# Kernel optimization log

Measured on AMD Instinct MI355X. Metric: run time of the kernel, lower is better.

Reference implementation:

```python
import jax, jax.numpy as jnp
import numpy as np

D = 1024
H = 16
DH = D // H
B = 8
T = 1024
EPS = 1e-5


def setup_inputs() -> dict:
    key = jax.random.key(0)
    ks = jax.random.split(key, 12)
    s = 0.02
    return {
        "x": jax.random.normal(ks[0], (B, T, D), dtype=jnp.float32),
        "ln1_scale": jnp.ones((D,), jnp.float32),
        "ln1_shift": jnp.zeros((D,), jnp.float32),
        "Wq": jax.random.normal(ks[1], (D, D), jnp.float32) * s,
        "Wk": jax.random.normal(ks[2], (D, D), jnp.float32) * s,
        "Wv": jax.random.normal(ks[3], (D, D), jnp.float32) * s,
        "Wo": jax.random.normal(ks[4], (D, D), jnp.float32) * s,
        "bo": jnp.zeros((D,), jnp.float32),
        "ln2_scale": jnp.ones((D,), jnp.float32),
        "ln2_shift": jnp.zeros((D,), jnp.float32),
        "W1": jax.random.normal(ks[5], (D, 4 * D), jnp.float32) * s,
        "b1": jnp.zeros((4 * D,), jnp.float32),
        "W2": jax.random.normal(ks[6], (4 * D, D), jnp.float32) * s,
        "b2": jnp.zeros((D,), jnp.float32),
    }


def _layernorm(x, scale, shift):
    mean = jnp.mean(x, axis=-1, keepdims=True)
    var = jnp.mean((x - mean) ** 2, axis=-1, keepdims=True)  # unbiased=False
    return (x - mean) * jax.lax.rsqrt(var + EPS) * scale + shift


def _gelu_tanh(x):
    c = jnp.sqrt(jnp.float32(2.0 / jnp.pi))
    return 0.5 * x * (1.0 + jnp.tanh(c * (x + 0.044715 * x ** 3)))


def reference(x, ln1_scale, ln1_shift, Wq, Wk, Wv, Wo, bo,
              ln2_scale, ln2_shift, W1, b1, W2, b2):
    b, t, d = x.shape
    x1 = _layernorm(x, ln1_scale, ln1_shift)
    # QKV projections (no bias), split heads -> (b, h, t, d_h)
    q = (x1 @ Wq).reshape(b, t, H, DH).transpose(0, 2, 1, 3)
    k = (x1 @ Wk).reshape(b, t, H, DH).transpose(0, 2, 1, 3)
    v = (x1 @ Wv).reshape(b, t, H, DH).transpose(0, 2, 1, 3)
    scores = jnp.einsum("bhqd,bhkd->bhqk", q, k) / jnp.sqrt(jnp.float32(DH))
    # original does tril then adds -inf upper-triangular mask -> standard causal mask
    causal = jnp.tril(jnp.ones((t, t), dtype=bool))
    scores = jnp.where(causal, scores, -jnp.inf)
    attn = jax.nn.softmax(scores, axis=-1)
    z = jnp.einsum("bhqk,bhkd->bhqd", attn, v)
    z = z.transpose(0, 2, 1, 3).reshape(b, t, d)
    x2 = z @ Wo + bo
    y = x2 + x
    y1 = _layernorm(y, ln2_scale, ln2_shift)
    y2 = _gelu_tanh(y1 @ W1 + b1) @ W2 + b2
    return y2 + y
```

## Files before the change

### kernel.cpp

```cpp
#include <hip/hip_runtime.h>

typedef unsigned short u16;
typedef __bf16 bf16x8 __attribute__((ext_vector_type(8)));
typedef float f32x4 __attribute__((ext_vector_type(4)));

#define D_MODEL 1024
#define NHEAD 16
#define DHEAD 64
#define BATCH 8
#define SEQ 1024
#define NROW 8192

__device__ __forceinline__ u16 f2bf(float f) {
  union { float f; unsigned int u; } a; a.f = f;
  unsigned int u = a.u;
  return (u16)((u + 0x7fffu + ((u >> 16) & 1u)) >> 16);
}

__device__ __forceinline__ float gelu_f(float x) {
  float y = 0.79788456080286535588f * (x + 0.044715f * x * x * x);
  return x / (1.0f + __expf(-2.0f * y));
}

__device__ __forceinline__ void async16(const void* gsrc, void* ldst) {
  __builtin_amdgcn_global_load_lds((__attribute__((address_space(1))) void*)gsrc,
                                   (__attribute__((address_space(3))) void*)ldst,
                                   16, 0, 0);
}

__global__ __launch_bounds__(256)
void wconv_kernel(const float* __restrict__ W, u16* __restrict__ WT, int K, int N) {
  __shared__ float tile[32][33];
  const int tx = threadIdx.x & 31, ty = threadIdx.x >> 5;
  const int n0 = blockIdx.x * 32, k0 = blockIdx.y * 32;
#pragma unroll
  for (int r = 0; r < 4; ++r)
    tile[ty + r * 8][tx] = W[(size_t)(k0 + ty + r * 8) * N + n0 + tx];
  __syncthreads();
#pragma unroll
  for (int r = 0; r < 4; ++r)
    WT[(size_t)(n0 + ty + r * 8) * K + k0 + tx] = f2bf(tile[tx][ty + r * 8]);
}

__global__ __launch_bounds__(256)
void ln_kernel(const float* __restrict__ x, const float* __restrict__ gamma,
               const float* __restrict__ beta, u16* __restrict__ out) {
  const int row = blockIdx.x, t = threadIdx.x;
  const float4 v = ((const float4*)(x + (size_t)row * D_MODEL))[t];
  float s  = v.x + v.y + v.z + v.w;
  float s2 = v.x * v.x + v.y * v.y + v.z * v.z + v.w * v.w;
#pragma unroll
  for (int off = 32; off >= 1; off >>= 1) {
    s  += __shfl_down(s, off);
    s2 += __shfl_down(s2, off);
  }
  __shared__ float red[8];
  const int w = t >> 6, l = t & 63;
  if (l == 0) { red[w] = s; red[4 + w] = s2; }
  __syncthreads();
  s  = red[0] + red[1] + red[2] + red[3];
  s2 = red[4] + red[5] + red[6] + red[7];
  const float mean = s * (1.0f / D_MODEL);
  const float var  = s2 * (1.0f / D_MODEL) - mean * mean;
  const float inv  = rsqrtf(var + 1e-5f);
  const float4 ga = ((const float4*)gamma)[t];
  const float4 be = ((const float4*)beta)[t];
  ushort4 ov;
  ov.x = f2bf((v.x - mean) * inv * ga.x + be.x);
  ov.y = f2bf((v.y - mean) * inv * ga.y + be.y);
  ov.z = f2bf((v.z - mean) * inv * ga.z + be.z);
  ov.w = f2bf((v.w - mean) * inv * ga.w + be.w);
  ((ushort4*)out)[(size_t)row * 256 + t] = ov;
}

#define MODE_QK 0
#define MODE_VT 1
#define MODE_F32_RES 2
#define MODE_GELU 3

template <int MODE>
__global__ __launch_bounds__(256, 2)
void gemm_bt(const u16* __restrict__ A, const u16* __restrict__ BT,
             const float* __restrict__ bias, const float* __restrict__ resid,
             void* __restrict__ outp, int M, int N, int K) {
  __shared__ u16 sA[2][128 * 32];
  __shared__ u16 sB[2][128 * 32];
  const int t = threadIdx.x;
  const int w = t >> 6, l = t & 63;
  const int c = l & 15, g = l >> 4;
  const int wr = w >> 1, wc = w & 1;
  const int bm = blockIdx.x, bn = blockIdx.y;

  f32x4 acc[4][4] = {};

  const char* Ab = (const char*)(A + (size_t)bm * 128 * K);
  const char* Bb = (const char*)(BT + (size_t)bn * 128 * K);
  const size_t ldb = (size_t)K * 2;
  const int srow = t >> 2;
  const int scolb = (t & 3) * 16;
  const int ldsoff = w * 1024;

  auto stage = [&](int buf, int k0) {
#pragma unroll
    for (int i = 0; i < 2; ++i) {
      async16(Ab + (size_t)(srow + i * 64) * ldb + (size_t)k0 * 2 + scolb,
              (char*)sA[buf] + i * 4096 + ldsoff);
      async16(Bb + (size_t)(srow + i * 64) * ldb + (size_t)k0 * 2 + scolb,
              (char*)sB[buf] + i * 4096 + ldsoff);
    }
  };

  stage(0, 0);
  asm volatile("s_waitcnt vmcnt(0)" ::: "memory");
  __builtin_amdgcn_s_barrier();

  const int nt = K >> 5;
  for (int it = 0; it < nt; ++it) {
    const int cur = it & 1;
    if (it + 1 < nt) stage(cur ^ 1, (it + 1) << 5);
    bf16x8 af[4], bfr[4];
#pragma unroll
    for (int m = 0; m < 4; ++m)
      af[m] = *(const bf16x8*)&sA[cur][(wr * 64 + m * 16 + c) * 32 + g * 8];
#pragma unroll
    for (int n = 0; n < 4; ++n)
      bfr[n] = *(const bf16x8*)&sB[cur][(wc * 64 + n * 16 + c) * 32 + g * 8];
#pragma unroll
    for (int m = 0; m < 4; ++m)
#pragma unroll
      for (int n = 0; n < 4; ++n)
        acc[m][n] = __builtin_amdgcn_mfma_f32_16x16x32_bf16(af[m], bfr[n], acc[m][n], 0, 0, 0);
    asm volatile("s_waitcnt vmcnt(0)" ::: "memory");
    __builtin_amdgcn_s_barrier();
  }

#pragma unroll
  for (int m = 0; m < 4; ++m) {
    const int r0 = bm * 128 + wr * 64 + m * 16 + g * 4;
#pragma unroll
    for (int n = 0; n < 4; ++n) {
      const int cc = bn * 128 + wc * 64 + n * 16 + c;
#pragma unroll
      for (int i = 0; i < 4; ++i) {
        const int r = r0 + i;
        const float v = acc[m][n][i];
        if constexpr (MODE == MODE_QK) {
          ((u16*)outp)[(((size_t)(r >> 10) * NHEAD + (cc >> 6)) * SEQ + (r & 1023)) * DHEAD + (cc & 63)] = f2bf(v);
        } else if constexpr (MODE == MODE_VT) {
          ((u16*)outp)[(((size_t)(r >> 10) * NHEAD + (cc >> 6)) * DHEAD + (cc & 63)) * SEQ + (r & 1023)] = f2bf(v);
        } else if constexpr (MODE == MODE_F32_RES) {
          const size_t idx = (size_t)r * N + cc;
          ((float*)outp)[idx] = v + bias[cc] + resid[idx];
        } else {
          const size_t idx = (size_t)r * N + cc;
          ((u16*)outp)[idx] = f2bf(gelu_f(v + bias[cc]));
        }
      }
    }
  }
}

__global__ __launch_bounds__(256, 3)
void attn_kernel(const u16* __restrict__ q, const u16* __restrict__ k,
                 const u16* __restrict__ vT, u16* __restrict__ z) {
  __shared__ u16 sK[2][64 * 64];
  __shared__ u16 sV[2][64 * 64];
  __shared__ u16 pb[4][32 * 64];

  const int t = threadIdx.x, w = t >> 6, l = t & 63;
  const int c = l & 15, g = l >> 4;
  const int bh = blockIdx.y;
  const int qb0 = blockIdx.x * 128;
  const int qw0 = qb0 + w * 32;

  const u16* qbase = q  + (size_t)bh * SEQ * DHEAD;
  const u16* kbase = k  + (size_t)bh * SEQ * DHEAD;
  const u16* vbase = vT + (size_t)bh * DHEAD * SEQ;

  bf16x8 qf[2][2];
#pragma unroll
  for (int j = 0; j < 2; ++j)
#pragma unroll
    for (int hh = 0; hh < 2; ++hh)
      qf[j][hh] = *(const bf16x8*)&qbase[(size_t)(qw0 + j * 16 + c) * DHEAD + hh * 32 + g * 8];

  f32x4 o[4][2] = {};
  float m[2]  = {-3.0e38f, -3.0e38f};
  float ls[2] = {0.0f, 0.0f};

  const int r8 = l >> 3, ch = l & 7;
  const int sw16 = (ch ^ r8) * 16;

  auto stage = [&](int buf, int kt) {
    const int kb0 = kt * 64;
#pragma unroll
    for (int i = 0; i < 2; ++i) {
      const int row = w * 8 + i * 32 + r8;
      async16((const char*)kbase + (size_t)(kb0 + row) * 128 + sw16,
              (char*)sK[buf] + w * 1024 + i * 4096);
      async16((const char*)vbase + (size_t)row * (SEQ * 2) + (size_t)kb0 * 2 + sw16,
              (char*)sV[buf] + w * 1024 + i * 4096);
    }
  };

  const int nkt = blockIdx.x * 2 + 2;
  stage(0, 0);

  for (int kt = 0; kt < nkt; ++kt) {
    const int cur = kt & 1;
    if (kt + 1 < nkt) {
      stage(cur ^ 1, kt + 1);
      asm volatile("s_waitcnt vmcnt(4)" ::: "memory");
    } else {
      asm volatile("s_waitcnt vmcnt(0)" ::: "memory");
    }
    __builtin_amdgcn_s_barrier();

    const int kb0 = kt * 64;
    if (kb0 < qw0 + 32) {
      const u16* sKc = sK[cur];
      const u16* sVc = sV[cur];
      const int cx = c & 7;

      f32x4 st[4][2];
#pragma unroll
      for (int s = 0; s < 4; ++s) {
        const int row = s * 16 + c;
        bf16x8 kf0 = *(const bf16x8*)&sKc[row * 64 + ((0 + g) ^ cx) * 8];
        bf16x8 kf1 = *(const bf16x8*)&sKc[row * 64 + ((4 + g) ^ cx) * 8];
#pragma unroll
        for (int j = 0; j < 2; ++j) {
          f32x4 z4 = {};
          z4 = __builtin_amdgcn_mfma_f32_16x16x32_bf16(kf0, qf[j][0], z4, 0, 0, 0);
          z4 = __builtin_amdgcn_mfma_f32_16x16x32_bf16(kf1, qf[j][1], z4, 0, 0, 0);
          st[s][j] = z4;
        }
      }

      const bool full = (kb0 + 64 <= qw0 + 1);
      float tmax[2] = {-3.0e38f, -3.0e38f};
#pragma unroll
      for (int s = 0; s < 4; ++s)
#pragma unroll
        for (int j = 0; j < 2; ++j)
#pragma unroll
          for (int i = 0; i < 4; ++i) {
            float vsc = st[s][j][i] * 0.125f;
            if (!full) {
              const int key = kb0 + s * 16 + g * 4 + i;
              vsc = (key <= qw0 + j * 16 + c) ? vsc : -1.0e30f;
            }
            st[s][j][i] = vsc;
            tmax[j] = fmaxf(tmax[j], vsc);
          }
#pragma unroll
      for (int j = 0; j < 2; ++j) {
        tmax[j] = fmaxf(tmax[j], __shfl_xor(tmax[j], 16));
        tmax[j] = fmaxf(tmax[j], __shfl_xor(tmax[j], 32));
      }
      float mnew[2], sc[2], psum[2];
#pragma unroll
      for (int j = 0; j < 2; ++j) {
        mnew[j] = fmaxf(m[j], tmax[j]);
        sc[j]   = __expf(m[j] - mnew[j]);
        psum[j] = 0.0f;
      }
#pragma unroll
      for (int s = 0; s < 4; ++s)
#pragma unroll
        for (int j = 0; j < 2; ++j)
#pragma unroll
          for (int i = 0; i < 4; ++i) {
            const float pv = __expf(st[s][j][i] - mnew[j]);
            st[s][j][i] = pv;
            psum[j] += pv;
          }
#pragma unroll
      for (int j = 0; j < 2; ++j) {
        psum[j] += __shfl_xor(psum[j], 16);
        psum[j] += __shfl_xor(psum[j], 32);
        ls[j] = ls[j] * sc[j] + psum[j];
        m[j]  = mnew[j];
#pragma unroll
        for (int d = 0; d < 4; ++d) o[d][j] = o[d][j] * sc[j];
      }

      u16* pw = pb[w];
#pragma unroll
      for (int s = 0; s < 4; ++s)
#pragma unroll
        for (int j = 0; j < 2; ++j) {
          const int row = j * 16 + c;
          const int swz = (s * 2 + (g >> 1)) ^ cx;
          ushort4 pv4;
          pv4.x = f2bf(st[s][j][0]); pv4.y = f2bf(st[s][j][1]);
          pv4.z = f2bf(st[s][j][2]); pv4.w = f2bf(st[s][j][3]);
          *(ushort4*)&pw[row * 64 + swz * 8 + (g & 1) * 4] = pv4;
        }

      bf16x8 pf[2][2];
#pragma unroll
      for (int j = 0; j < 2; ++j)
#pragma unroll
        for (int ks = 0; ks < 2; ++ks)
          pf[j][ks] = *(const bf16x8*)&pw[(j * 16 + c) * 64 + ((ks * 4 + g) ^ cx) * 8];

#pragma unroll
      for (int d = 0; d < 4; ++d) {
        const int vrow = d * 16 + c;
#pragma unroll
        for (int ks = 0; ks < 2; ++ks) {
          bf16x8 vf = *(const bf16x8*)&sVc[vrow * 64 + ((ks * 4 + g) ^ cx) * 8];
#pragma unroll
          for (int j = 0; j < 2; ++j)
            o[d][j] = __builtin_amdgcn_mfma_f32_16x16x32_bf16(vf, pf[j][ks], o[d][j], 0, 0, 0);
        }
      }
    }
    __builtin_amdgcn_s_barrier();
  }

  const int b = bh >> 4, h = bh & 15;
#pragma unroll
  for (int j = 0; j < 2; ++j) {
    const float inv = 1.0f / ls[j];
    const int qrow = qw0 + j * 16 + c;
    u16* zr = z + ((size_t)b * SEQ + qrow) * D_MODEL + h * DHEAD;
#pragma unroll
    for (int d = 0; d < 4; ++d) {
      ushort4 ov;
      ov.x = f2bf(o[d][j][0] * inv); ov.y = f2bf(o[d][j][1] * inv);
      ov.z = f2bf(o[d][j][2] * inv); ov.w = f2bf(o[d][j][3] * inv);
      *(ushort4*)&zr[d * 16 + g * 4] = ov;
    }
  }
}

extern "C" void kernel_launch(void* const* d_in, const int* in_sizes, int n_in,
                              void* d_out, int out_size, void* d_ws, size_t ws_size,
                              hipStream_t stream) {
  (void)in_sizes; (void)n_in; (void)out_size; (void)ws_size;
  const float* x   = (const float*)d_in[0];
  const float* g1  = (const float*)d_in[1];
  const float* s1  = (const float*)d_in[2];
  const float* Wq  = (const float*)d_in[3];
  const float* Wk  = (const float*)d_in[4];
  const float* Wv  = (const float*)d_in[5];
  const float* Wo  = (const float*)d_in[6];
  const float* bo  = (const float*)d_in[7];
  const float* g2  = (const float*)d_in[8];
  const float* s2  = (const float*)d_in[9];
  const float* W1  = (const float*)d_in[10];
  const float* b1  = (const float*)d_in[11];
  const float* W2  = (const float*)d_in[12];
  const float* b2  = (const float*)d_in[13];
  float* out = (float*)d_out;
  char* ws = (char*)d_ws;
  const size_t MB = 1024 * 1024;

  u16* wqT = (u16*)(ws + 0 * MB);
  u16* wkT = (u16*)(ws + 2 * MB);
  u16* wvT = (u16*)(ws + 4 * MB);
  u16* woT = (u16*)(ws + 6 * MB);
  u16* w1T = (u16*)(ws + 8 * MB);
  u16* w2T = (u16*)(ws + 16 * MB);
  u16* x1  = (u16*)(ws + 24 * MB);
  u16* qb  = (u16*)(ws + 40 * MB);
  u16* kb  = (u16*)(ws + 56 * MB);
  u16* vb  = (u16*)(ws + 72 * MB);
  u16* hb  = (u16*)(ws + 24 * MB);
  u16* zb  = (u16*)(ws + 88 * MB);
  u16* y1  = (u16*)(ws + 88 * MB);
  float* yb = (float*)(ws + 104 * MB);

  wconv_kernel<<<dim3(32, 32), 256, 0, stream>>>(Wq, wqT, 1024, 1024);
  wconv_kernel<<<dim3(32, 32), 256, 0, stream>>>(Wk, wkT, 1024, 1024);
  wconv_kernel<<<dim3(32, 32), 256, 0, stream>>>(Wv, wvT, 1024, 1024);
  wconv_kernel<<<dim3(32, 32), 256, 0, stream>>>(Wo, woT, 1024, 1024);
  wconv_kernel<<<dim3(128, 32), 256, 0, stream>>>(W1, w1T, 1024, 4096);
  wconv_kernel<<<dim3(32, 128), 256, 0, stream>>>(W2, w2T, 4096, 1024);
  ln_kernel<<<NROW, 256, 0, stream>>>(x, g1, s1, x1);
  gemm_bt<MODE_QK><<<dim3(64, 8), 256, 0, stream>>>(x1, wqT, nullptr, nullptr, qb, NROW, 1024, 1024);
  gemm_bt<MODE_QK><<<dim3(64, 8), 256, 0, stream>>>(x1, wkT, nullptr, nullptr, kb, NROW, 1024, 1024);
  gemm_bt<MODE_VT><<<dim3(64, 8), 256, 0, stream>>>(x1, wvT, nullptr, nullptr, vb, NROW, 1024, 1024);
  attn_kernel<<<dim3(8, 128), 256, 0, stream>>>(qb, kb, vb, zb);
  gemm_bt<MODE_F32_RES><<<dim3(64, 8), 256, 0, stream>>>(zb, woT, bo, x, yb, NROW, 1024, 1024);
  ln_kernel<<<NROW, 256, 0, stream>>>(yb, g2, s2, y1);
  gemm_bt<MODE_GELU><<<dim3(64, 32), 256, 0, stream>>>(y1, w1T, b1, nullptr, hb, NROW, 4096, 1024);
  gemm_bt<MODE_F32_RES><<<dim3(64, 8), 256, 0, stream>>>(hb, w2T, b2, yb, out, NROW, 1024, 4096);
}
```

Before: 404.2 us.

## Replace GEMM with 8-wave larger-tile swizzled kernel and fuse QKV projections

Replaces the 128x128, 4-wave GEMM with an 8-wave kernel. It uses 256-wide N tiles, a configurable M tile, a K-step of 64, XOR-swizzled LDS layout to avoid bank conflicts, s_setprio around MFMA bursts and an XCD-aware block remapping. The Q, K and V projections are merged into one GEMM over a concatenated weight buffer, so x1 is read once and there are fewer launches. The larger tiles raise data reuse and LDS footprint, which may reduce occupancy. Wo and W2 now launch only 256 workgroups, which risks underfilling the GPU.

New measurement: 463.2 us. 14.6% more time.

```diff
diff --git a/kernel.cpp b/kernel.cpp
--- a/kernel.cpp
+++ b/kernel.cpp
@@ -10,6 +10,8 @@
 #define BATCH 8
 #define SEQ 1024
 #define NROW 8192
+
+#define SBAR asm volatile("s_barrier" ::: "memory")
 
 __device__ __forceinline__ u16 f2bf(float f) {
   union { float f; unsigned int u; } a; a.f = f;
@@ -73,81 +75,132 @@
   ((ushort4*)out)[(size_t)row * 256 + t] = ov;
 }
 
-#define MODE_QK 0
-#define MODE_VT 1
+#define MODE_QKV 0
 #define MODE_F32_RES 2
 #define MODE_GELU 3
 
-template <int MODE>
-__global__ __launch_bounds__(256, 2)
-void gemm_bt(const u16* __restrict__ A, const u16* __restrict__ BT,
-             const float* __restrict__ bias, const float* __restrict__ resid,
-             void* __restrict__ outp, int M, int N, int K) {
-  __shared__ u16 sA[2][128 * 32];
-  __shared__ u16 sB[2][128 * 32];
-  const int t = threadIdx.x;
-  const int w = t >> 6, l = t & 63;
+template <int MODE, int MT>
+__global__ __launch_bounds__(512, 2)
+void gemm8(const u16* __restrict__ A, const u16* __restrict__ BT,
+           const float* __restrict__ bias, const float* __restrict__ resid,
+           void* __restrict__ outp, u16* __restrict__ out2, u16* __restrict__ out3,
+           int mtiles, int ntiles, int N, int K) {
+  constexpr int BM = MT * 32;
+  constexpr int P  = MT / 2;
+  constexpr int LA = BM / 64;
+  constexpr int LB = 4;
+  __shared__ u16 sA[2][BM * 64];
+  __shared__ u16 sB[2][256 * 64];
+
+  const int t = threadIdx.x, w = t >> 6, l = t & 63;
   const int c = l & 15, g = l >> 4;
-  const int wr = w >> 1, wc = w & 1;
-  const int bm = blockIdx.x, bn = blockIdx.y;
-
-  f32x4 acc[4][4] = {};
-
-  const char* Ab = (const char*)(A + (size_t)bm * 128 * K);
-  const char* Bb = (const char*)(BT + (size_t)bn * 128 * K);
-  const size_t ldb = (size_t)K * 2;
-  const int srow = t >> 2;
-  const int scolb = (t & 3) * 16;
-  const int ldsoff = w * 1024;
-
-  auto stage = [&](int buf, int k0) {
-#pragma unroll
-    for (int i = 0; i < 2; ++i) {
-      async16(Ab + (size_t)(srow + i * 64) * ldb + (size_t)k0 * 2 + scolb,
-              (char*)sA[buf] + i * 4096 + ldsoff);
-      async16(Bb + (size_t)(srow + i * 64) * ldb + (size_t)k0 * 2 + scolb,
-              (char*)sB[buf] + i * 4096 + ldsoff);
-    }
+  const int wr = w >> 2, wc = w & 3;
+
+  const int nwg = mtiles * ntiles;
+  const int orig = blockIdx.x;
+  const int wgid = (orig & 7) * (nwg >> 3) + (orig >> 3);
+  const int bm = wgid / ntiles, bn = wgid % ntiles;
+
+  const int ldb = K * 2;
+  const char* Ab = (const char*)A + (size_t)bm * BM * ldb;
+  const char* Bb = (const char*)BT + (size_t)bn * 256 * ldb;
+
+  int aoff[LA], boff[LB];
+#pragma unroll
+  for (int i = 0; i < LA; ++i) {
+    const int o = i * 512 + t, row = o >> 3, chg = (o & 7) ^ (row & 7);
+    aoff[i] = row * ldb + chg * 16;
+  }
+#pragma unroll
+  for (int i = 0; i < LB; ++i) {
+    const int o = i * 512 + t, row = o >> 3, chg = (o & 7) ^ (row & 7);
+    boff[i] = row * ldb + chg * 16;
+  }
+
+  auto stage = [&](int b, int k0) {
+    const int kb = k0 * 2;
+#pragma unroll
+    for (int i = 0; i < LA; ++i)
+      async16(Ab + (size_t)(aoff[i] + kb), (char*)sA[b] + (i * 512 + w * 64) * 16);
+#pragma unroll
+    for (int i = 0; i < LB; ++i)
+      async16(Bb + (size_t)(boff[i] + kb), (char*)sB[b] + (i * 512 + w * 64) * 16);
   };
+
+  auto ldA = [&](int cur, int mf, int ks) -> bf16x8 {
+    const int row = wr * (MT * 16) + mf * 16 + c;
+    return *(const bf16x8*)((const char*)sA[cur] + row * 128 + (((ks << 2) + g) ^ (row & 7)) * 16);
+  };
+  auto ldB = [&](int cur, int nf, int ks) -> bf16x8 {
+    const int row = wc * 64 + nf * 16 + c;
+    return *(const bf16x8*)((const char*)sB[cur] + row * 128 + (((ks << 2) + g) ^ (row & 7)) * 16);
+  };
+
+  f32x4 acc[MT][4] = {};
 
   stage(0, 0);
   asm volatile("s_waitcnt vmcnt(0)" ::: "memory");
-  __builtin_amdgcn_s_barrier();
-
-  const int nt = K >> 5;
+  SBAR;
+
+  const int nt = K >> 6;
   for (int it = 0; it < nt; ++it) {
     const int cur = it & 1;
-    if (it + 1 < nt) stage(cur ^ 1, (it + 1) << 5);
-    bf16x8 af[4], bfr[4];
-#pragma unroll
-    for (int m = 0; m < 4; ++m)
-      af[m] = *(const bf16x8*)&sA[cur][(wr * 64 + m * 16 + c) * 32 + g * 8];
-#pragma unroll
-    for (int n = 0; n < 4; ++n)
-      bfr[n] = *(const bf16x8*)&sB[cur][(wc * 64 + n * 16 + c) * 32 + g * 8];
-#pragma unroll
-    for (int m = 0; m < 4; ++m)
-#pragma unroll
-      for (int n = 0; n < 4; ++n)
-        acc[m][n] = __builtin_amdgcn_mfma_f32_16x16x32_bf16(af[m], bfr[n], acc[m][n], 0, 0, 0);
-    asm volatile("s_waitcnt vmcnt(0)" ::: "memory");
-    __builtin_amdgcn_s_barrier();
-  }
-
-#pragma unroll
-  for (int m = 0; m < 4; ++m) {
-    const int r0 = bm * 128 + wr * 64 + m * 16 + g * 4;
+    bf16x8 bfr[4][2];
+#pragma unroll
+    for (int p = 0; p < P; ++p) {
+      if (p == 0 && it + 1 < nt) stage(cur ^ 1, (it + 1) << 6);
+      bf16x8 af[2][2];
+#pragma unroll
+      for (int mi = 0; mi < 2; ++mi)
+#pragma unroll
+        for (int ks = 0; ks < 2; ++ks)
+          af[mi][ks] = ldA(cur, p * 2 + mi, ks);
+      if (p == 0) {
+#pragma unroll
+        for (int n = 0; n < 4; ++n)
+#pragma unroll
+          for (int ks = 0; ks < 2; ++ks)
+            bfr[n][ks] = ldB(cur, n, ks);
+      }
+      SBAR;
+      __builtin_amdgcn_s_setprio(1);
+#pragma unroll
+      for (int ks = 0; ks < 2; ++ks)
+#pragma unroll
+        for (int mi = 0; mi < 2; ++mi)
+#pragma unroll
+          for (int n = 0; n < 4; ++n)
+            acc[p * 2 + mi][n] = __builtin_amdgcn_mfma_f32_16x16x32_bf16(
+                af[mi][ks], bfr[n][ks], acc[p * 2 + mi][n], 0, 0, 0);
+      __builtin_amdgcn_s_setprio(0);
+      if (p + 1 < P) {
+        SBAR;
+      } else {
+        asm volatile("s_waitcnt vmcnt(0)" ::: "memory");
+        SBAR;
+      }
+    }
+  }
+
+#pragma unroll
+  for (int m = 0; m < MT; ++m) {
+    const int r0 = bm * BM + wr * (MT * 16) + m * 16 + g * 4;
 #pragma unroll
     for (int n = 0; n < 4; ++n) {
-      const int cc = bn * 128 + wc * 64 + n * 16 + c;
+      const int cc = bn * 256 + wc * 64 + n * 16 + c;
 #pragma unroll
       for (int i = 0; i < 4; ++i) {
         const int r = r0 + i;
         const float v = acc[m][n][i];
-        if constexpr (MODE == MODE_QK) {
-          ((u16*)outp)[(((size_t)(r >> 10) * NHEAD + (cc >> 6)) * SEQ + (r & 1023)) * DHEAD + (cc & 63)] = f2bf(v);
-        } else if constexpr (MODE == MODE_VT) {
-          ((u16*)outp)[(((size_t)(r >> 10) * NHEAD + (cc >> 6)) * DHEAD + (cc & 63)) * SEQ + (r & 1023)] = f2bf(v);
+        if constexpr (MODE == MODE_QKV) {
+          const int sel = cc >> 10, ccl = cc & 1023;
+          const int bb = r >> 10, tt = r & 1023, h = ccl >> 6, dh = ccl & 63;
+          if (sel == 0)
+            ((u16*)outp)[(((size_t)bb * NHEAD + h) * SEQ + tt) * DHEAD + dh] = f2bf(v);
+          else if (sel == 1)
+            out2[(((size_t)bb * NHEAD + h) * SEQ + tt) * DHEAD + dh] = f2bf(v);
+          else
+            out3[(((size_t)bb * NHEAD + h) * DHEAD + dh) * SEQ + tt] = f2bf(v);
         } else if constexpr (MODE == MODE_F32_RES) {
           const size_t idx = (size_t)r * N + cc;
           ((float*)outp)[idx] = v + bias[cc] + resid[idx];
@@ -358,9 +411,7 @@
   char* ws = (char*)d_ws;
   const size_t MB = 1024 * 1024;
 
-  u16* wqT = (u16*)(ws + 0 * MB);
-  u16* wkT = (u16*)(ws + 2 * MB);
-  u16* wvT = (u16*)(ws + 4 * MB);
+  u16* wqkvT = (u16*)(ws + 0 * MB);
   u16* woT = (u16*)(ws + 6 * MB);
   u16* w1T = (u16*)(ws + 8 * MB);
   u16* w2T = (u16*)(ws + 16 * MB);
@@ -373,19 +424,21 @@
   u16* y1  = (u16*)(ws + 88 * MB);
   float* yb = (float*)(ws + 104 * MB);
 
-  wconv_kernel<<<dim3(32, 32), 256, 0, stream>>>(Wq, wqT, 1024, 1024);
-  wconv_kernel<<<dim3(32, 32), 256, 0, stream>>>(Wk, wkT, 1024, 1024);
-  wconv_kernel<<<dim3(32, 32), 256, 0, stream>>>(Wv, wvT, 1024, 1024);
+  wconv_kernel<<<dim3(32, 32), 256, 0, stream>>>(Wq, wqkvT, 1024, 1024);
+  wconv_kernel<<<dim3(32, 32), 256, 0, stream>>>(Wk, wqkvT + 1024 * 1024, 1024, 1024);
+  wconv_kernel<<<dim3(32, 32), 256, 0, stream>>>(Wv, wqkvT + 2048 * 1024, 1024, 1024);
   wconv_kernel<<<dim3(32, 32), 256, 0, stream>>>(Wo, woT, 1024, 1024);
   wconv_kernel<<<dim3(128, 32), 256, 0, stream>>>(W1, w1T, 1024, 4096);
   wconv_kernel<<<dim3(32, 128), 256, 0, stream>>>(W2, w2T, 4096, 1024);
   ln_kernel<<<NROW, 256, 0, stream>>>(x, g1, s1, x1);
-  gemm_bt<MODE_QK><<<dim3(64, 8), 256, 0, stream>>>(x1, wqT, nullptr, nullptr, qb, NROW, 1024, 1024);
-  gemm_bt<MODE_QK><<<dim3(64, 8), 256, 0, stream>>>(x1, wkT, nullptr, nullptr, kb, NROW, 1024, 1024);
-  gemm_bt<MODE_VT><<<dim3(64, 8), 256, 0, stream>>>(x1, wvT, nullptr, nullptr, vb, NROW, 1024, 1024);
+  gemm8<MODE_QKV, 4><<<64 * 12, 512, 0, stream>>>(x1, wqkvT, nullptr, nullptr,
+                                                  qb, kb, vb, 64, 12, 3072, 1024);
   attn_kernel<<<dim3(8, 128), 256, 0, stream>>>(qb, kb, vb, zb);
-  gemm_bt<MODE_F32_RES><<<dim3(64, 8), 256, 0, stream>>>(zb, woT, bo, x, yb, NROW, 1024, 1024);
+  gemm8<MODE_F32_RES, 4><<<64 * 4, 512, 0, stream>>>(zb, woT, bo, x,
+                                                     yb, nullptr, nullptr, 64, 4, 1024, 1024);
   ln_kernel<<<NROW, 256, 0, stream>>>(yb, g2, s2, y1);
-  gemm_bt<MODE_GELU><<<dim3(64, 32), 256, 0, stream>>>(y1, w1T, b1, nullptr, hb, NROW, 4096, 1024);
-  gemm_bt<MODE_F32_RES><<<dim3(64, 8), 256, 0, stream>>>(hb, w2T, b2, yb, out, NROW, 1024, 4096);
-}
+  gemm8<MODE_GELU, 8><<<32 * 16, 512, 0, stream>>>(y1, w1T, b1, nullptr,
+                                                   hb, nullptr, nullptr, 32, 16, 4096, 1024);
+  gemm8<MODE_F32_RES, 4><<<64 * 4, 512, 0, stream>>>(hb, w2T, b2, yb,
+                                                     out, nullptr, nullptr, 64, 4, 1024, 4096);
+}
```

## Add 256x256-tile pipelined GEMM for the FFN up-projection

Applied to the files above, without the earlier changes.

Adds a new 512-thread GEMM kernel with 256x256 output tiles, 64-wide K steps, a four-slot LDS ring holding XOR-swizzled async loads, phase-interleaved staging with raised wave priority around the MFMAs, and an XCD-aware block remap. The FFN up-projection with GELU is switched to this kernel, aiming for more operand reuse and better overlap of loads with matrix math. The existing gemm_bt launch bound is also raised to 4 blocks per CU, which may limit registers for its 64 accumulators and risk spills.

Result: no change. 406.5 us (+0.6%).

```diff
diff --git a/kernel.cpp b/kernel.cpp
--- a/kernel.cpp
+++ b/kernel.cpp
@@ -79,7 +79,7 @@
 #define MODE_GELU 3
 
 template <int MODE>
-__global__ __launch_bounds__(256, 2)
+__global__ __launch_bounds__(256, 4)
 void gemm_bt(const u16* __restrict__ A, const u16* __restrict__ BT,
              const float* __restrict__ bias, const float* __restrict__ resid,
              void* __restrict__ outp, int M, int N, int K) {
@@ -149,6 +149,135 @@
         } else if constexpr (MODE == MODE_VT) {
           ((u16*)outp)[(((size_t)(r >> 10) * NHEAD + (cc >> 6)) * DHEAD + (cc & 63)) * SEQ + (r & 1023)] = f2bf(v);
         } else if constexpr (MODE == MODE_F32_RES) {
+          const size_t idx = (size_t)r * N + cc;
+          ((float*)outp)[idx] = v + bias[cc] + resid[idx];
+        } else {
+          const size_t idx = (size_t)r * N + cc;
+          ((u16*)outp)[idx] = f2bf(gelu_f(v + bias[cc]));
+        }
+      }
+    }
+  }
+}
+
+#define GPHASE(KT, Q, STAGE_STMT, DOWAIT)                                   \
+  {                                                                         \
+    const int aslot_ = (2 * (KT) + wr) & 3;                                 \
+    bf16x8 af_[2][2];                                                       \
+    _Pragma("unroll")                                                       \
+    for (int mi = 0; mi < 2; ++mi)                                          \
+      _Pragma("unroll")                                                     \
+      for (int ks = 0; ks < 2; ++ks) {                                      \
+        const int row_ = (Q) * 32 + mi * 16 + c;                            \
+        af_[mi][ks] = *(const bf16x8*)((const char*)sA[aslot_]              \
+            + row_ * 128 + ((((ks << 2) + g) ^ cx) * 16));                  \
+      }                                                                     \
+    if ((Q) == 0) {                                                         \
+      const int bslot_ = (2 * (KT) + (wc >> 1)) & 3;                        \
+      _Pragma("unroll")                                                     \
+      for (int n = 0; n < 4; ++n)                                           \
+        _Pragma("unroll")                                                   \
+        for (int ks = 0; ks < 2; ++ks) {                                    \
+          const int row_ = (wc & 1) * 64 + n * 16 + c;                      \
+          bfr[n][ks] = *(const bf16x8*)((const char*)sB[bslot_]             \
+              + row_ * 128 + ((((ks << 2) + g) ^ cx) * 16));                \
+        }                                                                   \
+    }                                                                       \
+    STAGE_STMT;                                                             \
+    if (DOWAIT) asm volatile("s_waitcnt vmcnt(4)" ::: "memory");            \
+    __builtin_amdgcn_s_barrier();                                           \
+    asm volatile("s_waitcnt lgkmcnt(0)" ::: "memory");                      \
+    __builtin_amdgcn_s_setprio(1);                                          \
+    _Pragma("unroll")                                                       \
+    for (int ks = 0; ks < 2; ++ks)                                          \
+      _Pragma("unroll")                                                     \
+      for (int mi = 0; mi < 2; ++mi)                                        \
+        _Pragma("unroll")                                                   \
+        for (int n = 0; n < 4; ++n)                                         \
+          acc[(Q) * 2 + mi][n] = __builtin_amdgcn_mfma_f32_16x16x32_bf16(   \
+              af_[mi][ks], bfr[n][ks], acc[(Q) * 2 + mi][n], 0, 0, 0);      \
+    __builtin_amdgcn_s_setprio(0);                                          \
+    __builtin_amdgcn_s_barrier();                                           \
+  }
+
+template <int MODE>
+__global__ __launch_bounds__(512, 2)
+void gemm256(const u16* __restrict__ A, const u16* __restrict__ BT,
+             const float* __restrict__ bias, const float* __restrict__ resid,
+             void* __restrict__ outp, int mtiles, int ntiles, int N, int K) {
+  __shared__ u16 sA[4][128 * 64];
+  __shared__ u16 sB[4][128 * 64];
+
+  const int t = threadIdx.x, w = t >> 6, l = t & 63;
+  const int c = l & 15, g = l >> 4, cx = c & 7;
+  const int wr = w >> 2, wc = w & 3;
+
+  const int nwg = mtiles * ntiles;
+  const int orig = blockIdx.x;
+  const int wgid = (orig & 7) * (nwg >> 3) + (orig >> 3);
+  const int bm = wgid / ntiles, bn = wgid % ntiles;
+
+  const int ldb = K * 2;
+  const char* Ab = (const char*)A + (size_t)bm * 256 * ldb;
+  const char* Bb = (const char*)BT + (size_t)bn * 256 * ldb;
+
+  auto stageA = [&](int k, int h) {
+    char* dst = (char*)sA[(2 * k + h) & 3];
+    const char* src = Ab + (size_t)(h * 128) * ldb + (size_t)k * 128;
+#pragma unroll
+    for (int i = 0; i < 2; ++i) {
+      const int o = i * 512 + t, row = o >> 3, ch = (o & 7) ^ (row & 7);
+      async16(src + (size_t)row * ldb + ch * 16, dst + o * 16);
+    }
+  };
+  auto stageB = [&](int k, int h) {
+    char* dst = (char*)sB[(2 * k + h) & 3];
+    const char* src = Bb + (size_t)(h * 128) * ldb + (size_t)k * 128;
+#pragma unroll
+    for (int i = 0; i < 2; ++i) {
+      const int o = i * 512 + t, row = o >> 3, ch = (o & 7) ^ (row & 7);
+      async16(src + (size_t)row * ldb + ch * 16, dst + o * 16);
+    }
+  };
+
+  f32x4 acc[8][4] = {};
+  bf16x8 bfr[4][2];
+
+  const int nt = K >> 6;
+  stageA(0, 0); stageA(0, 1);
+  stageB(0, 0); stageB(0, 1);
+  stageB(1, 0); stageB(1, 1);
+  asm volatile("s_waitcnt vmcnt(4)" ::: "memory");
+  __builtin_amdgcn_s_barrier();
+
+  const int nj = nt >> 1;
+  for (int j = 0; j < nj; ++j) {
+    const int k0 = 2 * j, k1 = 2 * j + 1;
+    const int nlast = nt - 1;
+    const int t2 = (k0 + 2 > nlast) ? nlast : k0 + 2;
+    const int t3 = (k1 + 2 > nlast) ? nlast : k1 + 2;
+    GPHASE(k0, 0, stageA(k1, 0), false);
+    GPHASE(k0, 1, stageA(k1, 1), false);
+    GPHASE(k0, 2, stageB(t2, 0), false);
+    GPHASE(k0, 3, stageB(t2, 1), true);
+    GPHASE(k1, 0, stageA(t2, 0), false);
+    GPHASE(k1, 1, stageA(t2, 1), false);
+    GPHASE(k1, 2, stageB(t3, 0), false);
+    GPHASE(k1, 3, stageB(t3, 1), true);
+  }
+  asm volatile("s_waitcnt vmcnt(0)" ::: "memory");
+
+#pragma unroll
+  for (int m = 0; m < 8; ++m) {
+    const int r0 = bm * 256 + wr * 128 + m * 16 + g * 4;
+#pragma unroll
+    for (int n = 0; n < 4; ++n) {
+      const int cc = bn * 256 + wc * 64 + n * 16 + c;
+#pragma unroll
+      for (int i = 0; i < 4; ++i) {
+        const int r = r0 + i;
+        const float v = acc[m][n][i];
+        if constexpr (MODE == MODE_F32_RES) {
           const size_t idx = (size_t)r * N + cc;
           ((float*)outp)[idx] = v + bias[cc] + resid[idx];
         } else {
@@ -386,6 +515,8 @@
   attn_kernel<<<dim3(8, 128), 256, 0, stream>>>(qb, kb, vb, zb);
   gemm_bt<MODE_F32_RES><<<dim3(64, 8), 256, 0, stream>>>(zb, woT, bo, x, yb, NROW, 1024, 1024);
   ln_kernel<<<NROW, 256, 0, stream>>>(yb, g2, s2, y1);
-  gemm_bt<MODE_GELU><<<dim3(64, 32), 256, 0, stream>>>(y1, w1T, b1, nullptr, hb, NROW, 4096, 1024);
-  gemm_bt<MODE_F32_RES><<<dim3(64, 8), 256, 0, stream>>>(hb, w2T, b2, yb, out, NROW, 1024, 4096);
-}
+  gemm256<MODE_GELU><<<32 * 16, 512, 0, stream>>>(y1, w1T, b1, nullptr,
+                                                  hb, 32, 16, 4096, 1024);
+  gemm_bt<MODE_F32_RES><<<dim3(64, 8), 256, 0, stream>>>(hb, w2T, b2, yb,
+                                                         out, NROW, 1024, 4096);
+}
```
